# Kernel optimization log

Measured on AMD Instinct MI355X. Metric: run time of the kernel, lower is better.

## Reference

```python
import jax, jax.numpy as jnp
import numpy as np

IMAGE_SIZE = 256
PSIZE = 8
STRIDE = 4
WINDOW = IMAGE_SIZE + 1 - PSIZE  # 249


def _build_indices():
    # replicate image2patch.__init__ mask construction
    cur = np.arange(0, WINDOW, STRIDE)
    if cur[-1] != WINDOW - 1:
        cur = np.append(cur, WINDOW - 1)
    grid = np.arange(WINDOW * WINDOW).reshape(WINDOW, WINDOW)
    mask = grid[np.ix_(cur, cur)].reshape(-1)  # [M] window-origin flat indices
    rows = mask // WINDOW  # [M] patch top-left row
    cols = mask % WINDOW   # [M] patch top-left col
    k = np.arange(PSIZE * PSIZE)
    di, dj = k // PSIZE, k % PSIZE  # offsets within patch; flat index k = i*PSIZE + j
    r_full = rows[:, None] + di[None, :]  # [M, PSIZE^2]
    c_full = cols[:, None] + dj[None, :]  # [M, PSIZE^2]
    return jnp.asarray(r_full, dtype=jnp.int32), jnp.asarray(c_full, dtype=jnp.int32)

R_IDX, C_IDX = _build_indices()


def setup_inputs() -> dict:
    key = jax.random.key(0)
    x = jax.random.normal(key, (32, 8, IMAGE_SIZE, IMAGE_SIZE), dtype=jnp.float32)
    return {"input_data": x}


def reference(input_data):
    # output[b*c, m, i*PSIZE+j] = input_data[b, c, rows[m]+i, cols[m]+j]
    B, C, H, W = input_data.shape
    x = input_data.reshape(B * C, H, W)
    out = x[:, R_IDX, C_IDX]  # [B*C, M, PSIZE^2] vectorized sliding-window gather
    return out
```

## Files before the change

kernel.cpp:

```cpp
#include <hip/hip_runtime.h>


constexpr unsigned NPDIM   = 63;
constexpr unsigned PATCHES = NPDIM * NPDIM;
constexpr unsigned CHUNKS  = 16;
constexpr unsigned ROWPAD  = 65;

__global__ __launch_bounds__(256) void image2patch_kernel(
    const float4* __restrict__ in4, float4* __restrict__ out4) {
    __shared__ float4 lds4[8 * ROWPAD];

    unsigned bid = blockIdx.x;
    unsigned n   = bid / NPDIM;
    unsigned pr  = bid - n * NPDIM;

    unsigned inbase4 = n * 16384u + pr * 256u;
    unsigned t = threadIdx.x;
    {
        unsigned r0 = t >> 6, c0 = t & 63u;
        lds4[r0 * ROWPAD + c0] = in4[inbase4 + t];
        unsigned i1 = t + 256u;
        unsigned r1 = i1 >> 6, c1 = i1 & 63u;
        lds4[r1 * ROWPAD + c1] = in4[inbase4 + i1];
    }
    __syncthreads();

    unsigned outbase4 = (n * PATCHES + pr * NPDIM) * CHUNKS;
    #pragma unroll
    for (unsigned it = 0; it < 4; ++it) {
        unsigned i = it * 256u + t;
        if (i < NPDIM * CHUNKS) {
            unsigned pc  = i >> 4;
            unsigned k4  = i & 15u;
            unsigned di  = k4 >> 1;
            unsigned dj4 = k4 & 1u;
            out4[outbase4 + i] = lds4[di * ROWPAD + pc + dj4];
        }
    }
}

extern "C" void kernel_launch(void* const* d_in, const int* in_sizes, int n_in,
                              void* d_out, int out_size, void* d_ws, size_t ws_size,
                              hipStream_t stream) {
    const float4* in4 = (const float4*)d_in[0];
    float4* out4 = (float4*)d_out;
    unsigned blocks = 256u * NPDIM;
    image2patch_kernel<<<blocks, 256, 0, stream>>>(in4, out4);
}
```

Baseline: 298.2 us.

## Process several patch-row bands per block with double-buffered LDS and prefetch

Each block now handles 8 consecutive patch-row bands instead of one. The next band's global loads are issued into registers before the current band is written out, and two LDS buffers alternate so one barrier per band is enough. This aims to hide global load latency behind the output stores and to cut block launch overhead. In exchange the grid is 8x smaller, so fewer waves are in flight, and each loop iteration still waits on a barrier.

```diff
diff --git a/kernel.cpp b/kernel.cpp
--- a/kernel.cpp
+++ b/kernel.cpp
@@ -5,36 +5,54 @@
 constexpr unsigned PATCHES = NPDIM * NPDIM;
 constexpr unsigned CHUNKS  = 16;
 constexpr unsigned ROWPAD  = 65;
+constexpr unsigned BANDS   = 256u * NPDIM;
+constexpr unsigned BPB     = 8;
+constexpr unsigned BLOCKS  = BANDS / BPB;
 
-__global__ __launch_bounds__(256) void image2patch_kernel(
+__global__ __launch_bounds__(256, 8) void image2patch_kernel(
     const float4* __restrict__ in4, float4* __restrict__ out4) {
-    __shared__ float4 lds4[8 * ROWPAD];
+    __shared__ float4 lds[2][8 * ROWPAD];
 
-    unsigned bid = blockIdx.x;
-    unsigned n   = bid / NPDIM;
-    unsigned pr  = bid - n * NPDIM;
+    unsigned t = threadIdx.x;
+    unsigned band0 = blockIdx.x * BPB;
 
-    unsigned inbase4 = n * 16384u + pr * 256u;
-    unsigned t = threadIdx.x;
-    {
-        unsigned r0 = t >> 6, c0 = t & 63u;
-        lds4[r0 * ROWPAD + c0] = in4[inbase4 + t];
-        unsigned i1 = t + 256u;
-        unsigned r1 = i1 >> 6, c1 = i1 & 63u;
-        lds4[r1 * ROWPAD + c1] = in4[inbase4 + i1];
-    }
-    __syncthreads();
+    unsigned r0 = t >> 6, c0 = t & 63u;
+    unsigned i1 = t + 256u;
+    unsigned r1 = i1 >> 6, c1 = i1 & 63u;
 
-    unsigned outbase4 = (n * PATCHES + pr * NPDIM) * CHUNKS;
-    #pragma unroll
-    for (unsigned it = 0; it < 4; ++it) {
-        unsigned i = it * 256u + t;
-        if (i < NPDIM * CHUNKS) {
-            unsigned pc  = i >> 4;
-            unsigned k4  = i & 15u;
-            unsigned di  = k4 >> 1;
-            unsigned dj4 = k4 & 1u;
-            out4[outbase4 + i] = lds4[di * ROWPAD + pc + dj4];
+    unsigned n  = band0 / NPDIM;
+    unsigned pr = band0 - n * NPDIM;
+    unsigned inbase = n * 16384u + pr * 256u;
+    float4 v0 = in4[inbase + t];
+    float4 v1 = in4[inbase + 256u + t];
+
+    for (unsigned i = 0; i < BPB; ++i) {
+        unsigned buf = i & 1u;
+        lds[buf][r0 * ROWPAD + c0] = v0;
+        lds[buf][r1 * ROWPAD + c1] = v1;
+        unsigned outbase = (n * PATCHES + pr * NPDIM) * CHUNKS;
+        __syncthreads();
+
+        if (i + 1 < BPB) {
+            unsigned nb  = band0 + i + 1;
+            unsigned nn  = nb / NPDIM;
+            unsigned npr = nb - nn * NPDIM;
+            unsigned nin = nn * 16384u + npr * 256u;
+            v0 = in4[nin + t];
+            v1 = in4[nin + 256u + t];
+            n = nn; pr = npr;
+        }
+
+        #pragma unroll
+        for (unsigned it = 0; it < 4; ++it) {
+            unsigned idx = it * 256u + t;
+            if (idx < NPDIM * CHUNKS) {
+                unsigned pc  = idx >> 4;
+                unsigned k4  = idx & 15u;
+                unsigned di  = k4 >> 1;
+                unsigned dj4 = k4 & 1u;
+                out4[outbase + idx] = lds[buf][di * ROWPAD + pc + dj4];
+            }
         }
     }
 }
@@ -44,6 +62,5 @@
                               hipStream_t stream) {
     const float4* in4 = (const float4*)d_in[0];
     float4* out4 = (float4*)d_out;
-    unsigned blocks = 256u * NPDIM;
-    image2patch_kernel<<<blocks, 256, 0, stream>>>(in4, out4);
+    image2patch_kernel<<<BLOCKS, 256, 0, stream>>>(in4, out4);
 }
```

After: 316.1 us. +6.0%, slower.
